# Kernel optimization log

Hardware: AMD Instinct MI355X
Metric: run time of the kernel (lower is better)

Reference implementation:

```python
import jax, jax.numpy as jnp
import numpy as np

B, L, H, NH, T, WIN = 4, 4096, 256, 8, 64, 16
D = H // NH
NEG_SLOPE = 5.0
MASK_FILL = -1e12


def _leaky(x):
    return jnp.where(x >= 0, x, NEG_SLOPE * x)


def _window_indices():
    # static numpy index construction, mirrors EdgeBlock.self_attn
    off_u = np.concatenate([np.zeros(WIN + 1, np.int64), np.arange(1, WIN + 1)])
    off_d = np.concatenate([np.arange(-WIN, 0), np.zeros(WIN + 1, np.int64)])
    idx_u = np.arange(L)[:, None] + off_u  # [L, 2W+1]
    idx_d = np.arange(L)[:, None] + off_d  # [L, 2W+1]
    idx_mask = (idx_d >= 0) & (idx_u < L)
    return idx_u % L, idx_d % L, idx_mask


def setup_inputs() -> dict:
    key = jax.random.key(0)
    ks = jax.random.split(key, 12)
    s = 1.0 / np.sqrt(H)
    lengths = jnp.array([L, L - 128, L - 512, L - 1024])
    context_mask = jnp.arange(L)[None, :] < lengths[:, None]  # [B, L] bool
    return {
        'context': jax.random.normal(ks[0], (B, L, H), jnp.float32),
        'types': jax.random.normal(ks[1], (B, T, H), jnp.float32),
        'context_mask': context_mask,
        'W_types': jax.random.normal(ks[2], (H, H), jnp.float32) * s,
        'b_types': jnp.zeros((H,), jnp.float32),
        'W_context': jax.random.normal(ks[3], (H, H), jnp.float32) * s,
        'b_context': jnp.zeros((H,), jnp.float32),
        'upon': jax.random.normal(ks[4], (NH, D), jnp.float32) * s,
        'down': jax.random.normal(ks[5], (NH, D), jnp.float32) * s,
        'cross': jax.random.normal(ks[6], (NH, D, D), jnp.float32) * s,
        'W_out': jax.random.normal(ks[7], (H, H), jnp.float32) * s,
        'b_out': jnp.zeros((H,), jnp.float32),
    }


def reference(context, types, context_mask, W_types, b_types, W_context, b_context,
              upon, down, cross, W_out, b_out):
    idx_u, idx_d, idx_mask = _window_indices()

    # head-split projections
    types_h = (types @ W_types + b_types).reshape(B, T, NH, D)      # [B,T,n,d]
    context_h = (context @ W_context + b_context).reshape(B, L, NH, D)  # [B,L,n,d]

    # ---- cross attention scores: context queries over types (EdgeBlock.cross_attn)
    upon_q = jnp.einsum('blnd,nd->bnl', context_h, upon)
    down_t = jnp.einsum('btnd,nd->bnt', types_h, down)
    concat_ct = upon_q[..., None] + down_t[:, :, None, :]           # [B,n,L,T]
    prod_ct = jnp.einsum('blnd,ndh,btnh->bnlt', context_h, cross, types_h)
    types_s = _leaky(concat_ct + prod_ct)                            # [B,n,L,T]

    # ---- windowed self attention scores (EdgeBlock.self_attn)
    down_s = jnp.einsum('blnd,nd->bnl', context_h, down)
    concat_self = upon_q[:, :, idx_u] + down_s[:, :, idx_d]          # [B,n,L,2W+1]
    win_idx = idx_u  # source: cat([indices_d[:, :0], indices_u[:, 0:]]) == indices_u
    wmask = context_mask[:, win_idx] & idx_mask                      # [B,L,2W+1]
    value_h = context_h[:, win_idx]                                  # [B,L,2W+1,n,d]
    prod_self = jnp.einsum('blnd,ndh,blvnh->bnlv', context_h, cross, value_h)
    context_s = jnp.where(wmask[:, None], _leaky(concat_self + prod_self), MASK_FILL)

    # ---- joint softmax over types + window, then aggregate
    weights = jax.nn.softmax(jnp.concatenate([types_s, context_s], axis=-1), axis=-1)
    types_w, context_w = weights[..., :T], weights[..., T:]
    upd_t = jnp.einsum('bnlt,btnd->blnd', types_w, types_h)
    upd_c = jnp.einsum('bnlv,blvnd->blnd', context_w, value_h)
    update = (upd_t + upd_c).reshape(B, L, H)

    # residual + output transform (no_gate=True path: Linear + Tanh)
    return jnp.tanh((update + context) @ W_out + b_out)
```

## Files before the change

kernel.cpp:

```cpp
#include <hip/hip_runtime.h>
#include <cstdint>

#define Bq 4
#define Lq 4096
#define Hq 256
#define NHq 8
#define Tq 64
#define WINq 16
#define Dq 32
#define NSLOTS 33
#define NEG_SLOPE 5.0f
#define MASK_FILL -1e12f
#define TLq 64
#define MB 16

typedef __attribute__((ext_vector_type(8))) short short8;
typedef __attribute__((ext_vector_type(4))) float f32x4;

__device__ __forceinline__ float leaky(float x) { return x >= 0.f ? x : NEG_SLOPE * x; }

__device__ __forceinline__ uint16_t f2bf(float x) {
    uint32_t u = __float_as_uint(x);
    uint32_t r = (u + 0x7fffu + ((u >> 16) & 1u)) >> 16;
    return (uint16_t)r;
}
__device__ __forceinline__ float bf2f(uint16_t h) {
    return __uint_as_float(((uint32_t)h) << 16);
}

__global__ void k_prep(const float* __restrict__ Wc, const float* __restrict__ Wo,
                       uint16_t* __restrict__ pc_hi, uint16_t* __restrict__ pc_lo,
                       uint16_t* __restrict__ po_hi, uint16_t* __restrict__ po_lo,
                       const float* __restrict__ types, const float* __restrict__ Wt,
                       const float* __restrict__ bt, const float* __restrict__ down,
                       float* __restrict__ types_h, float* __restrict__ types_hT,
                       float* __restrict__ down_t) {
    __shared__ float sin[Hq];
    __shared__ float outr[Hq];
    if (blockIdx.x < 128) {
        int wsel = blockIdx.x >> 6;
        int blk = blockIdx.x & 63;
        const float* W = wsel ? Wo : Wc;
        uint16_t* ph = wsel ? po_hi : pc_hi;
        uint16_t* pl = wsel ? po_lo : pc_lo;
        int base = blk * 1024;
        for (int idx = base + threadIdx.x; idx < base + 1024; idx += 256) {
            int j = idx & 7, l = (idx >> 3) & 63, fragi = idx >> 9;
            int kc = fragi & 7, nt = fragi >> 3;
            int k = kc * 32 + (l >> 4) * 8 + j;
            int c = nt * 16 + (l & 15);
            float x = W[k * Hq + c];
            uint16_t h = f2bf(x);
            ph[idx] = h;
            pl[idx] = f2bf(x - bf2f(h));
        }
        return;
    }
    int row = blockIdx.x - 128;
    int h = threadIdx.x;
    int b = row >> 6, t = row & 63;
    sin[h] = types[(size_t)row * Hq + h];
    __syncthreads();
    float acc = bt[h];
    for (int k = 0; k < Hq; k += 4) {
        float4 iv = *(const float4*)&sin[k];
        acc = fmaf(iv.x, Wt[(k + 0) * Hq + h], acc);
        acc = fmaf(iv.y, Wt[(k + 1) * Hq + h], acc);
        acc = fmaf(iv.z, Wt[(k + 2) * Hq + h], acc);
        acc = fmaf(iv.w, Wt[(k + 3) * Hq + h], acc);
    }
    types_h[(size_t)row * Hq + h] = acc;
    types_hT[(size_t)(b * Hq + h) * Tq + t] = acc;
    outr[h] = acc;
    __syncthreads();
    if (h < NHq) {
        float s = 0.f;
        for (int d = 0; d < Dq; ++d) s += outr[h * Dq + d] * down[h * Dq + d];
        down_t[(b * NHq + h) * Tq + t] = s;
    }
}

#define APAD 264
#define OPAD 258
__global__ void __launch_bounds__(256) k_ctx(
        const float* __restrict__ ctx,
        const uint16_t* __restrict__ wp_hi, const uint16_t* __restrict__ wp_lo,
        const float* __restrict__ bc, const float* __restrict__ upon,
        const float* __restrict__ down,
        float* __restrict__ ctx_hT, float* __restrict__ uq,
        float* __restrict__ dsv) {
    int row0 = blockIdx.x * MB;
    int b = row0 >> 12, l0 = row0 & (Lq - 1);
    int tid = threadIdx.x;
    int w = tid >> 6, l = tid & 63;
    __shared__ __align__(16) char smem_raw[MB * APAD * 4];
    uint16_t* a_hi = (uint16_t*)smem_raw;
    uint16_t* a_lo = a_hi + MB * APAD;
    float* outb = (float*)smem_raw;

    {
        const float4* src = (const float4*)(ctx + (size_t)row0 * Hq);
#pragma unroll
        for (int j = 0; j < 4; ++j) {
            int f = tid + j * 256;
            int r = f >> 6, cg = f & 63;
            float4 v = src[f];
            uint16_t h0 = f2bf(v.x), h1 = f2bf(v.y), h2 = f2bf(v.z), h3 = f2bf(v.w);
            ushort4 hh = {h0, h1, h2, h3};
            ushort4 ll = {f2bf(v.x - bf2f(h0)), f2bf(v.y - bf2f(h1)),
                          f2bf(v.z - bf2f(h2)), f2bf(v.w - bf2f(h3))};
            *(ushort4*)&a_hi[r * APAD + cg * 4] = hh;
            *(ushort4*)&a_lo[r * APAD + cg * 4] = ll;
        }
    }
    __syncthreads();

    int nt0 = w * 4;
    int m = l & 15, quad = l >> 4;
    f32x4 acc[4];
#pragma unroll
    for (int t = 0; t < 4; ++t) acc[t] = (f32x4){0.f, 0.f, 0.f, 0.f};
#pragma unroll
    for (int kc = 0; kc < 8; ++kc) {
        short8 ah = *(const short8*)&a_hi[m * APAD + kc * 32 + quad * 8];
        short8 al = *(const short8*)&a_lo[m * APAD + kc * 32 + quad * 8];
#pragma unroll
        for (int t = 0; t < 4; ++t) {
            int fragi = (nt0 + t) * 8 + kc;
            short8 wh = *(const short8*)&wp_hi[fragi * 512 + l * 8];
            short8 wl = *(const short8*)&wp_lo[fragi * 512 + l * 8];
            acc[t] = __builtin_amdgcn_mfma_f32_16x16x32_bf16(ah, wh, acc[t], 0, 0, 0);
            acc[t] = __builtin_amdgcn_mfma_f32_16x16x32_bf16(ah, wl, acc[t], 0, 0, 0);
            acc[t] = __builtin_amdgcn_mfma_f32_16x16x32_bf16(al, wh, acc[t], 0, 0, 0);
        }
    }
    __syncthreads();

#pragma unroll
    for (int t = 0; t < 4; ++t) {
        int col = (nt0 + t) * 16 + m;
        float bv = bc[col];
#pragma unroll
        for (int r = 0; r < 4; ++r)
            outb[(quad * 4 + r) * OPAD + col] = acc[t][r] + bv;
    }
    __syncthreads();

    if (tid < MB * NHq) {
        int r = tid >> 3, n = tid & 7;
        float su = 0.f, sd = 0.f;
        for (int d = 0; d < Dq; ++d) {
            float v = outb[r * OPAD + n * Dq + d];
            su += v * upon[n * Dq + d];
            sd += v * down[n * Dq + d];
        }
        uq[(b * NHq + n) * Lq + l0 + r] = su;
        dsv[(b * NHq + n) * Lq + l0 + r] = sd;
    }
    {
        float* dst = ctx_hT + (size_t)(b * Hq + tid) * Lq + l0;
#pragma unroll
        for (int j = 0; j < MB / 4; ++j) {
            float4 o;
            o.x = outb[(4 * j + 0) * OPAD + tid];
            o.y = outb[(4 * j + 1) * OPAD + tid];
            o.z = outb[(4 * j + 2) * OPAD + tid];
            o.w = outb[(4 * j + 3) * OPAD + tid];
            ((float4*)dst)[j] = o;
        }
    }
}

__global__ void __launch_bounds__(256) k_attn(
        const float* __restrict__ ctx_hT, const float* __restrict__ types_h,
        const float* __restrict__ types_hT, const float* __restrict__ cross,
        const float* __restrict__ uq, const float* __restrict__ dsv,
        const float* __restrict__ dt, const unsigned char* __restrict__ maskp,
        float* __restrict__ update) {
    int blk = blockIdx.x;
    int lt = blk & 63, n = (blk >> 6) & 7, b = blk >> 9;
    int l0 = lt * TLq;
    int tid = threadIdx.x;
    int ls = tid >> 2;
    int q  = tid & 3;
    int pl = l0 + ls;
    bool mask_b8 = (maskp[1] != 0);

    __shared__ float chx_s[32 * 97];
    __shared__ float crs_s[32 * 36];
    __shared__ float cr_s[64 * 36];
    __shared__ float dots_s[64 * 19];
    __shared__ float tts_s[32 * 64];
    __shared__ float tts2_s[64 * 36 + 16];
    __shared__ float uqe[96], dsve[96], maskf[96], dts[64];

    {
        int d = tid >> 3, k = tid & 7;
        const float* grow = ctx_hT + ((size_t)(b * NHq + n) * Dq + d) * Lq;
        float* lrow = &chx_s[d * 97 + k * 12];
        if (l0 >= 16 && l0 <= Lq - 80) {
            const float4* g = (const float4*)(grow + (l0 - 16) + k * 12);
            float4 v0 = g[0], v1 = g[1], v2 = g[2];
            lrow[0] = v0.x; lrow[1] = v0.y; lrow[2]  = v0.z; lrow[3]  = v0.w;
            lrow[4] = v1.x; lrow[5] = v1.y; lrow[6]  = v1.z; lrow[7]  = v1.w;
            lrow[8] = v2.x; lrow[9] = v2.y; lrow[10] = v2.z; lrow[11] = v2.w;
        } else {
#pragma unroll
            for (int m = 0; m < 12; ++m) {
                int gl = l0 - 16 + k * 12 + m;
                int glw = (gl < 0) ? gl + Lq : ((gl >= Lq) ? gl - Lq : gl);
                lrow[m] = grow[glw];
            }
        }
    }
    {
        float4 v = ((const float4*)(cross + n * (Dq * Dq)))[tid];
        float* p = &crs_s[(tid >> 3) * 36 + (tid & 7) * 4];
        p[0] = v.x; p[1] = v.y; p[2] = v.z; p[3] = v.w;
    }
    {
        const float4* src = (const float4*)(types_hT + (size_t)(b * NHq + n) * Dq * Tq);
        float4* dst = (float4*)tts_s;
        dst[tid] = src[tid];
        dst[tid + 256] = src[tid + 256];
    }
    {
        int t = tid >> 2, c4 = tid & 3;
        const float4* src = (const float4*)(types_h + (size_t)(b * Tq + t) * Hq
                                            + n * Dq + 8 * c4);
        float* p = &tts2_s[t * 36 + 4 * (t >> 4) + 8 * c4];
        ((float4*)p)[0] = src[0];
        ((float4*)p)[1] = src[1];
    }
    if (tid < 96) {
        int gl = l0 - 16 + tid;
        int glw = (gl < 0) ? gl + Lq : ((gl >= Lq) ? gl - Lq : gl);
        uqe[tid] = uq[(b * NHq + n) * Lq + glw];
        unsigned char mb = mask_b8 ? maskp[b * Lq + glw]
                                   : maskp[(size_t)(b * Lq + glw) * 4];
        maskf[tid] = mb ? 1.f : 0.f;
    } else if (tid < 192) {
        int j = tid - 96;
        int gl = l0 - 16 + j;
        int glw = (gl < 0) ? gl + Lq : ((gl >= Lq) ? gl - Lq : gl);
        dsve[j] = dsv[(b * NHq + n) * Lq + glw];
    } else {
        dts[tid - 192] = dt[(b * NHq + n) * Tq + (tid - 192)];
    }
    __syncthreads();

    {
        float a[8];
#pragma unroll
        for (int ii = 0; ii < 8; ++ii) a[ii] = 0.f;
#pragma unroll 2
        for (int d = 0; d < Dq; ++d) {
            float chv = chx_s[d * 97 + ls + 16];
            const float4* cp = (const float4*)(&crs_s[d * 36 + 8 * q]);
            float4 c0 = cp[0], c1 = cp[1];
            a[0] = fmaf(chv, c0.x, a[0]); a[1] = fmaf(chv, c0.y, a[1]);
            a[2] = fmaf(chv, c0.z, a[2]); a[3] = fmaf(chv, c0.w, a[3]);
            a[4] = fmaf(chv, c1.x, a[4]); a[5] = fmaf(chv, c1.y, a[5]);
            a[6] = fmaf(chv, c1.z, a[6]); a[7] = fmaf(chv, c1.w, a[7]);
        }
        float4* wp = (float4*)(&cr_s[ls * 36 + 8 * q]);
        wp[0] = make_float4(a[0], a[1], a[2], a[3]);
        wp[1] = make_float4(a[4], a[5], a[6], a[7]);
    }

    float dot_self;
    {
        float cv8[8];
#pragma unroll
        for (int k = 0; k < 8; ++k) cv8[k] = cr_s[ls * 36 + 8 * q + k];
#pragma unroll
        for (int u = 0; u < 17; ++u) {
            float a = 0.f;
#pragma unroll
            for (int k = 0; k < 8; ++k)
                a = fmaf(cv8[k], chx_s[(8 * q + k) * 97 + ls + 16 + u], a);
            a += __shfl_xor(a, 1);
            a += __shfl_xor(a, 2);
            if (u == 0) dot_self = a;
            else if (q == 0) dots_s[ls * 19 + u] = a;
        }
    }

    float uq_l = uqe[ls + 16];
    float dsv_l = dsve[ls + 16];
    float cmask = maskf[ls + 16];

    int tb = 16 * q;
    float st[16];
#pragma unroll
    for (int j = 0; j < 16; ++j) st[j] = 0.f;
#pragma unroll 2
    for (int d = 0; d < Dq; ++d) {
        float cv = cr_s[ls * 36 + d];
        const float4* r4 = (const float4*)&tts_s[d * 64 + tb];
        float4 r0 = r4[0], r1 = r4[1], r2 = r4[2], r3 = r4[3];
        st[0]  = fmaf(cv, r0.x, st[0]);  st[1]  = fmaf(cv, r0.y, st[1]);
        st[2]  = fmaf(cv, r0.z, st[2]);  st[3]  = fmaf(cv, r0.w, st[3]);
        st[4]  = fmaf(cv, r1.x, st[4]);  st[5]  = fmaf(cv, r1.y, st[5]);
        st[6]  = fmaf(cv, r1.z, st[6]);  st[7]  = fmaf(cv, r1.w, st[7]);
        st[8]  = fmaf(cv, r2.x, st[8]);  st[9]  = fmaf(cv, r2.y, st[9]);
        st[10] = fmaf(cv, r2.z, st[10]); st[11] = fmaf(cv, r2.w, st[11]);
        st[12] = fmaf(cv, r3.x, st[12]); st[13] = fmaf(cv, r3.y, st[13]);
        st[14] = fmaf(cv, r3.z, st[14]); st[15] = fmaf(cv, r3.w, st[15]);
    }
#pragma unroll
    for (int j = 0; j < 16; ++j)
        st[j] = leaky(uq_l + dts[tb + j] + st[j]);

    int nv = (q == 0) ? 5 : 4;
    float su[4];
#pragma unroll
    for (int j = 0; j < 4; ++j) {
        int u = q + 1 + 4 * j;
        bool ok = (pl + u < Lq) && (maskf[ls + 16 + u] > 0.5f);
        su[j] = ok ? leaky(uqe[ls + 16 + u] + dsv_l + dots_s[ls * 19 + u])
                   : MASK_FILL;
    }

    float m = st[0];
#pragma unroll
    for (int j = 1; j < 16; ++j) m = fmaxf(m, st[j]);
#pragma unroll
    for (int j = 0; j < 5; ++j) {
        if (j < nv) {
            int v = q + 4 * j;
            if ((pl + v >= 16) && (cmask > 0.5f))
                m = fmaxf(m, leaky(uq_l + dsve[ls + v] + dot_self));
        }
    }
#pragma unroll
    for (int j = 0; j < 4; ++j) m = fmaxf(m, su[j]);
    m = fmaxf(m, __shfl_xor(m, 1));
    m = fmaxf(m, __shfl_xor(m, 2));
    float sum = 0.f, wself = 0.f;
#pragma unroll
    for (int j = 0; j < 16; ++j) { st[j] = __expf(st[j] - m); sum += st[j]; }
#pragma unroll
    for (int j = 0; j < 5; ++j) {
        if (j < nv) {
            int v = q + 4 * j;
            if ((pl + v >= 16) && (cmask > 0.5f)) {
                float e = __expf(leaky(uq_l + dsve[ls + v] + dot_self) - m);
                wself += e; sum += e;
            }
        }
    }
#pragma unroll
    for (int j = 0; j < 4; ++j)  { su[j] = __expf(su[j] - m); sum += su[j]; }
    sum += __shfl_xor(sum, 1);
    sum += __shfl_xor(sum, 2);
    float inv = 1.f / sum;
#pragma unroll
    for (int j = 0; j < 16; ++j) st[j] *= inv;
    wself *= inv;
#pragma unroll
    for (int j = 0; j < 4; ++j)  su[j] *= inv;

    float* dstrow = update + (size_t)(b * Lq + pl) * Hq + n * Dq;
#pragma unroll
    for (int c = 0; c < 4; ++c) {
        float u8[8];
#pragma unroll
        for (int e = 0; e < 8; ++e) u8[e] = 0.f;
#pragma unroll 2
        for (int j = 0; j < 16; ++j) {
            const float* vp = &tts2_s[(tb + j) * 36 + 4 * q + 8 * c];
            float4 a0 = ((const float4*)vp)[0];
            float4 a1 = ((const float4*)vp)[1];
            float wt = st[j];
            u8[0] = fmaf(wt, a0.x, u8[0]); u8[1] = fmaf(wt, a0.y, u8[1]);
            u8[2] = fmaf(wt, a0.z, u8[2]); u8[3] = fmaf(wt, a0.w, u8[3]);
            u8[4] = fmaf(wt, a1.x, u8[4]); u8[5] = fmaf(wt, a1.y, u8[5]);
            u8[6] = fmaf(wt, a1.z, u8[6]); u8[7] = fmaf(wt, a1.w, u8[7]);
        }
#pragma unroll
        for (int e = 0; e < 8; ++e)
            u8[e] = fmaf(wself, chx_s[(8 * c + e) * 97 + ls + 16], u8[e]);
#pragma unroll
        for (int j = 0; j < 4; ++j) {
            float wu = su[j];
            int u = q + 1 + 4 * j;
#pragma unroll
            for (int e = 0; e < 8; ++e)
                u8[e] = fmaf(wu, chx_s[(8 * c + e) * 97 + ls + 16 + u], u8[e]);
        }
#pragma unroll
        for (int e = 0; e < 8; ++e) {
            u8[e] += __shfl_xor(u8[e], 1);
            u8[e] += __shfl_xor(u8[e], 2);
        }
        if (q == c) {
            ((float4*)(dstrow + 8 * c))[0] = make_float4(u8[0], u8[1], u8[2], u8[3]);
            ((float4*)(dstrow + 8 * c))[1] = make_float4(u8[4], u8[5], u8[6], u8[7]);
        }
    }
}

__global__ void __launch_bounds__(256) k_out(
        const float* __restrict__ update, const float* __restrict__ ctx,
        const uint16_t* __restrict__ wp_hi, const uint16_t* __restrict__ wp_lo,
        const float* __restrict__ bo, float* __restrict__ out) {
    int row0 = blockIdx.x * MB;
    int tid = threadIdx.x;
    int w = tid >> 6, l = tid & 63;
    __shared__ __align__(16) char smem_raw[MB * APAD * 4];
    uint16_t* a_hi = (uint16_t*)smem_raw;
    uint16_t* a_lo = a_hi + MB * APAD;

    {
        const float4* s0 = (const float4*)(update + (size_t)row0 * Hq);
        const float4* s1 = (const float4*)(ctx + (size_t)row0 * Hq);
#pragma unroll
        for (int j = 0; j < 4; ++j) {
            int f = tid + j * 256;
            int r = f >> 6, cg = f & 63;
            float4 a = s0[f], bv = s1[f];
            float4 v; v.x = a.x + bv.x; v.y = a.y + bv.y;
            v.z = a.z + bv.z; v.w = a.w + bv.w;
            uint16_t h0 = f2bf(v.x), h1 = f2bf(v.y), h2 = f2bf(v.z), h3 = f2bf(v.w);
            ushort4 hh = {h0, h1, h2, h3};
            ushort4 ll = {f2bf(v.x - bf2f(h0)), f2bf(v.y - bf2f(h1)),
                          f2bf(v.z - bf2f(h2)), f2bf(v.w - bf2f(h3))};
            *(ushort4*)&a_hi[r * APAD + cg * 4] = hh;
            *(ushort4*)&a_lo[r * APAD + cg * 4] = ll;
        }
    }
    __syncthreads();

    int nt0 = w * 4;
    int m = l & 15, quad = l >> 4;
    f32x4 acc[4];
#pragma unroll
    for (int t = 0; t < 4; ++t) acc[t] = (f32x4){0.f, 0.f, 0.f, 0.f};
#pragma unroll
    for (int kc = 0; kc < 8; ++kc) {
        short8 ah = *(const short8*)&a_hi[m * APAD + kc * 32 + quad * 8];
        short8 al = *(const short8*)&a_lo[m * APAD + kc * 32 + quad * 8];
#pragma unroll
        for (int t = 0; t < 4; ++t) {
            int fragi = (nt0 + t) * 8 + kc;
            short8 wh = *(const short8*)&wp_hi[fragi * 512 + l * 8];
            short8 wl = *(const short8*)&wp_lo[fragi * 512 + l * 8];
            acc[t] = __builtin_amdgcn_mfma_f32_16x16x32_bf16(ah, wh, acc[t], 0, 0, 0);
            acc[t] = __builtin_amdgcn_mfma_f32_16x16x32_bf16(ah, wl, acc[t], 0, 0, 0);
            acc[t] = __builtin_amdgcn_mfma_f32_16x16x32_bf16(al, wh, acc[t], 0, 0, 0);
        }
    }
#pragma unroll
    for (int t = 0; t < 4; ++t) {
        int col = (nt0 + t) * 16 + m;
        float bv = bo[col];
#pragma unroll
        for (int r = 0; r < 4; ++r)
            out[(size_t)(row0 + quad * 4 + r) * Hq + col] = tanhf(acc[t][r] + bv);
    }
}

extern "C" void kernel_launch(void* const* d_in, const int* in_sizes, int n_in,
                              void* d_out, int out_size, void* d_ws, size_t ws_size,
                              hipStream_t stream) {
    const float* context   = (const float*)d_in[0];
    const float* types     = (const float*)d_in[1];
    const unsigned char* cmask = (const unsigned char*)d_in[2];
    const float* W_types   = (const float*)d_in[3];
    const float* b_types   = (const float*)d_in[4];
    const float* W_context = (const float*)d_in[5];
    const float* b_context = (const float*)d_in[6];
    const float* upon      = (const float*)d_in[7];
    const float* down      = (const float*)d_in[8];
    const float* cross     = (const float*)d_in[9];
    const float* W_out     = (const float*)d_in[10];
    const float* b_out     = (const float*)d_in[11];
    float* out = (float*)d_out;
    float* ws  = (float*)d_ws;

    float* ctx_hT   = ws;
    float* update   = ws + 4194304;
    uint16_t* wcp_hi = (uint16_t*)(ws + 8388608);
    uint16_t* wcp_lo = wcp_hi + 65536;
    uint16_t* wop_hi = wcp_hi + 131072;
    uint16_t* wop_lo = wcp_hi + 196608;

    float* types_h  = out;
    float* types_hT = out + 65536;
    float* down_t   = out + 131072;
    float* uqp      = out + 133120;
    float* dsvp     = out + 264192;

    k_prep<<<128 + Bq * Tq, 256, 0, stream>>>(W_context, W_out,
                                              wcp_hi, wcp_lo, wop_hi, wop_lo,
                                              types, W_types, b_types, down,
                                              types_h, types_hT, down_t);
    k_ctx<<<Bq * Lq / MB, 256, 0, stream>>>(context, wcp_hi, wcp_lo, b_context,
                                            upon, down, ctx_hT, uqp, dsvp);
    k_attn<<<Bq * NHq * (Lq / TLq), 256, 0, stream>>>(ctx_hT, types_h, types_hT, cross,
                                                      uqp, dsvp, down_t, cmask, update);
    k_out<<<Bq * Lq / MB, 256, 0, stream>>>(update, context, wop_hi, wop_lo, b_out, out);
}
```

Baseline: 183.3 us.

## Keep cross-projected rows in registers via shuffles and drop two LDS buffers

Removes the cr_s and tts_s shared-memory arrays. The per-row cross-projected vector now stays in registers and is exchanged across the 4-lane group with __shfl, and the type-score product reads the existing tts2_s layout instead of a transposed copy. This cuts LDS footprint and global loads of types_hT, and launch_bounds now asks for 5 blocks per CU to raise occupancy. In exchange it adds shuffle instructions, changes the LDS access pattern in the score loop, and may cause register pressure or spills under the tighter bound.

Measured after the change: 190.0 us. +3.7%, slower.

```diff
diff --git a/kernel.cpp b/kernel.cpp
--- a/kernel.cpp
+++ b/kernel.cpp
@@ -171,7 +171,7 @@
     }
 }
 
-__global__ void __launch_bounds__(256) k_attn(
+__global__ void __launch_bounds__(256, 5) k_attn(
         const float* __restrict__ ctx_hT, const float* __restrict__ types_h,
         const float* __restrict__ types_hT, const float* __restrict__ cross,
         const float* __restrict__ uq, const float* __restrict__ dsv,
@@ -188,9 +188,7 @@
 
     __shared__ float chx_s[32 * 97];
     __shared__ float crs_s[32 * 36];
-    __shared__ float cr_s[64 * 36];
     __shared__ float dots_s[64 * 19];
-    __shared__ float tts_s[32 * 64];
     __shared__ float tts2_s[64 * 36 + 16];
     __shared__ float uqe[96], dsve[96], maskf[96], dts[64];
 
@@ -217,12 +215,6 @@
         float4 v = ((const float4*)(cross + n * (Dq * Dq)))[tid];
         float* p = &crs_s[(tid >> 3) * 36 + (tid & 7) * 4];
         p[0] = v.x; p[1] = v.y; p[2] = v.z; p[3] = v.w;
-    }
-    {
-        const float4* src = (const float4*)(types_hT + (size_t)(b * NHq + n) * Dq * Tq);
-        float4* dst = (float4*)tts_s;
-        dst[tid] = src[tid];
-        dst[tid + 256] = src[tid + 256];
     }
     {
         int t = tid >> 2, c4 = tid & 3;
@@ -249,40 +241,32 @@
     }
     __syncthreads();
 
-    {
-        float a[8];
-#pragma unroll
-        for (int ii = 0; ii < 8; ++ii) a[ii] = 0.f;
+    float a[8];
+#pragma unroll
+    for (int ii = 0; ii < 8; ++ii) a[ii] = 0.f;
 #pragma unroll 2
-        for (int d = 0; d < Dq; ++d) {
-            float chv = chx_s[d * 97 + ls + 16];
-            const float4* cp = (const float4*)(&crs_s[d * 36 + 8 * q]);
-            float4 c0 = cp[0], c1 = cp[1];
-            a[0] = fmaf(chv, c0.x, a[0]); a[1] = fmaf(chv, c0.y, a[1]);
-            a[2] = fmaf(chv, c0.z, a[2]); a[3] = fmaf(chv, c0.w, a[3]);
-            a[4] = fmaf(chv, c1.x, a[4]); a[5] = fmaf(chv, c1.y, a[5]);
-            a[6] = fmaf(chv, c1.z, a[6]); a[7] = fmaf(chv, c1.w, a[7]);
-        }
-        float4* wp = (float4*)(&cr_s[ls * 36 + 8 * q]);
-        wp[0] = make_float4(a[0], a[1], a[2], a[3]);
-        wp[1] = make_float4(a[4], a[5], a[6], a[7]);
+    for (int d = 0; d < Dq; ++d) {
+        float chv = chx_s[d * 97 + ls + 16];
+        const float4* cp = (const float4*)(&crs_s[d * 36 + 8 * q]);
+        float4 c0 = cp[0], c1 = cp[1];
+        a[0] = fmaf(chv, c0.x, a[0]); a[1] = fmaf(chv, c0.y, a[1]);
+        a[2] = fmaf(chv, c0.z, a[2]); a[3] = fmaf(chv, c0.w, a[3]);
+        a[4] = fmaf(chv, c1.x, a[4]); a[5] = fmaf(chv, c1.y, a[5]);
+        a[6] = fmaf(chv, c1.z, a[6]); a[7] = fmaf(chv, c1.w, a[7]);
     }
 
     float dot_self;
     {
-        float cv8[8];
-#pragma unroll
-        for (int k = 0; k < 8; ++k) cv8[k] = cr_s[ls * 36 + 8 * q + k];
 #pragma unroll
         for (int u = 0; u < 17; ++u) {
-            float a = 0.f;
+            float acc = 0.f;
 #pragma unroll
             for (int k = 0; k < 8; ++k)
-                a = fmaf(cv8[k], chx_s[(8 * q + k) * 97 + ls + 16 + u], a);
-            a += __shfl_xor(a, 1);
-            a += __shfl_xor(a, 2);
-            if (u == 0) dot_self = a;
-            else if (q == 0) dots_s[ls * 19 + u] = a;
+                acc = fmaf(a[k], chx_s[(8 * q + k) * 97 + ls + 16 + u], acc);
+            acc += __shfl_xor(acc, 1);
+            acc += __shfl_xor(acc, 2);
+            if (u == 0) dot_self = acc;
+            else if (q == 0) dots_s[ls * 19 + u] = acc;
         }
     }
 
@@ -294,19 +278,26 @@
     float st[16];
 #pragma unroll
     for (int j = 0; j < 16; ++j) st[j] = 0.f;
-#pragma unroll 2
-    for (int d = 0; d < Dq; ++d) {
-        float cv = cr_s[ls * 36 + d];
-        const float4* r4 = (const float4*)&tts_s[d * 64 + tb];
-        float4 r0 = r4[0], r1 = r4[1], r2 = r4[2], r3 = r4[3];
-        st[0]  = fmaf(cv, r0.x, st[0]);  st[1]  = fmaf(cv, r0.y, st[1]);
-        st[2]  = fmaf(cv, r0.z, st[2]);  st[3]  = fmaf(cv, r0.w, st[3]);
-        st[4]  = fmaf(cv, r1.x, st[4]);  st[5]  = fmaf(cv, r1.y, st[5]);
-        st[6]  = fmaf(cv, r1.z, st[6]);  st[7]  = fmaf(cv, r1.w, st[7]);
-        st[8]  = fmaf(cv, r2.x, st[8]);  st[9]  = fmaf(cv, r2.y, st[9]);
-        st[10] = fmaf(cv, r2.z, st[10]); st[11] = fmaf(cv, r2.w, st[11]);
-        st[12] = fmaf(cv, r3.x, st[12]); st[13] = fmaf(cv, r3.y, st[13]);
-        st[14] = fmaf(cv, r3.z, st[14]); st[15] = fmaf(cv, r3.w, st[15]);
+#pragma unroll
+    for (int half = 0; half < 2; ++half) {
+        float crf[16];
+#pragma unroll
+        for (int k = 0; k < 16; ++k)
+            crf[k] = __shfl(a[k & 7], 2 * half + (k >> 3), 4);
+#pragma unroll 4
+        for (int j = 0; j < 16; ++j) {
+            const float4* rp =
+                (const float4*)&tts2_s[(tb + j) * 36 + 4 * q + 16 * half];
+            float4 v0 = rp[0], v1 = rp[1], v2 = rp[2], v3 = rp[3];
+            st[j] = fmaf(crf[0],  v0.x, st[j]); st[j] = fmaf(crf[1],  v0.y, st[j]);
+            st[j] = fmaf(crf[2],  v0.z, st[j]); st[j] = fmaf(crf[3],  v0.w, st[j]);
+            st[j] = fmaf(crf[4],  v1.x, st[j]); st[j] = fmaf(crf[5],  v1.y, st[j]);
+            st[j] = fmaf(crf[6],  v1.z, st[j]); st[j] = fmaf(crf[7],  v1.w, st[j]);
+            st[j] = fmaf(crf[8],  v2.x, st[j]); st[j] = fmaf(crf[9],  v2.y, st[j]);
+            st[j] = fmaf(crf[10], v2.z, st[j]); st[j] = fmaf(crf[11], v2.w, st[j]);
+            st[j] = fmaf(crf[12], v3.x, st[j]); st[j] = fmaf(crf[13], v3.y, st[j]);
+            st[j] = fmaf(crf[14], v3.z, st[j]); st[j] = fmaf(crf[15], v3.w, st[j]);
+        }
     }
 #pragma unroll
     for (int j = 0; j < 16; ++j)
```
